# Kernel optimization log

Measured on AMD Instinct MI355X. Metric: run time of the kernel, lower is better.

## Reference

```python
import jax, jax.numpy as jnp
import numpy as np
import math

TOTAL_HEADS = 16
CONTEXTUAL_HEADS = 4


def _compute_slopes(heads):
    def slopes_power_of_2(n):
        start = 2 ** (-2 ** (-(math.log2(n) - 3)))
        ratio = start
        return [start * ratio ** i for i in range(n)]
    if math.log2(heads).is_integer():
        return slopes_power_of_2(heads)
    closest = 2 ** math.floor(math.log2(heads))
    return slopes_power_of_2(closest) + slopes_power_of_2(2 * closest)[0::2][: heads - closest]


def setup_inputs() -> dict:
    key = jax.random.key(0)
    kq, kk = jax.random.split(key)
    b, h, s, d = 1, 16, 2048, 64
    q = jax.random.normal(kq, (b, h, s, d), dtype=jnp.float32)
    k = jax.random.normal(kk, (b, h, s, d), dtype=jnp.float32)
    cross_attn_bias = jnp.zeros((TOTAL_HEADS, 1, 1), dtype=jnp.float32)
    return {"q": q, "k": k, "cross_attn_bias": cross_attn_bias,
            "i": s, "j": s, "offset": 0, "prefix": 16}


def reference(q, k, cross_attn_bias, i, j, offset, prefix):
    b = q.shape[0]
    ch = CONTEXTUAL_HEADS
    slopes = jnp.asarray(_compute_slopes(TOTAL_HEADS), dtype=jnp.float32).reshape(-1, 1, 1)  # [H,1,1]

    # base distance bias: -|j - i|, shape [i, j]
    i_arange = jnp.arange(offset, i + offset)
    j_arange = jnp.arange(j)
    bias = -jnp.abs(j_arange[None, :] - i_arange[:, None]).astype(jnp.float32)

    # contextual heads: data-dependent bias with bidirectional cumsum
    qc = q[:, :ch]
    kc = k[:, :ch]
    dots = jnp.einsum('bhid,bhjd->bhij', qc, kc) * (qc.shape[-1] ** -0.5)
    c_bias = -jax.nn.sigmoid(dots)  # [b, ch, i, j]
    upper = jnp.triu(jnp.ones((i, j), dtype=bool), offset + 1)
    lower = jnp.tril(jnp.ones((i, j), dtype=bool), offset - 1)
    c_up = jnp.cumsum(jnp.where(upper, c_bias, 0.0), axis=-1)
    c_lo = jnp.flip(jnp.cumsum(jnp.flip(jnp.where(lower, c_bias, 0.0), axis=-1), axis=-1), axis=-1)
    c_pos = c_up + c_lo  # [b, ch, i, j]

    bias_full = jnp.concatenate(
        [c_pos, jnp.broadcast_to(bias, (b, TOTAL_HEADS - ch, i, j))], axis=1)  # [b, H, i, j]

    attn_bias = slopes * bias_full  # symmetric path

    # prefix cross-attention bias
    is_prefix = jnp.arange(j) < prefix
    is_cross = (is_prefix[:, None] ^ is_prefix[None, :])[offset:]  # [i, j]
    attn_bias = jnp.where(is_cross, cross_attn_bias, attn_bias)
    return attn_bias
```

## Files before the change

kernel.cpp:

```cpp
#include <hip/hip_runtime.h>
#include <hip/hip_bf16.h>

typedef __bf16 bf16_t;
typedef bf16_t bf16x8 __attribute__((ext_vector_type(8)));
typedef float f32x4 __attribute__((ext_vector_type(4)));
typedef unsigned long long u64_t;

#define TH 16
#define CH 4
#define DD 64
#define SJ 2048
#define SP (SJ + 4)
#define RROWS 8
#define KT (SJ/16)
#define NCTX (CH*SJ/RROWS)
#define AROWS 16
#define NALIBI ((TH-CH)*SJ/AROWS)
#define NBLK (NCTX + NALIBI)
#define WSK_BYTES ((size_t)CH*KT*2*64*16)

__device__ __forceinline__ float sigmoidf_(float x) {
    return __builtin_amdgcn_rcpf(1.0f + __expf(-x));
}

__device__ __forceinline__ float bsel(u64_t u, int e) {
    return __uint_as_float((((unsigned int)(u >> (16 * e)) & 0xffffu) << 16));
}

__global__ __launch_bounds__(256) void prep_kernel(
    const float* __restrict__ k, bf16_t* __restrict__ wsk)
{
    const int t    = (int)blockIdx.x * 256 + (int)threadIdx.x;
    const int h    = t >> 14;
    const int ct   = (t >> 7) & 127;
    const int kk   = (t >> 6) & 1;
    const int lane = t & 63;
    const int col  = ct * 16 + (lane & 15);
    const int db   = kk * 32 + (lane >> 4) * 8;
    const float* p = k + ((size_t)h * SJ + col) * DD + db;
    f32x4 v0 = *(const f32x4*)p;
    f32x4 v1 = *(const f32x4*)(p + 4);
    bf16x8 o;
    #pragma unroll
    for (int e = 0; e < 4; ++e) { o[e] = (bf16_t)v0[e]; o[e + 4] = (bf16_t)v1[e]; }
    *(bf16x8*)(wsk + (size_t)t * 8) = o;
}

__global__ __launch_bounds__(512, 4) void fused_kernel(
    const float* __restrict__ q, const float* __restrict__ k,
    const bf16_t* __restrict__ wsk, int use_ws,
    const float* __restrict__ cab, const int* __restrict__ offp,
    const int* __restrict__ prep, float* __restrict__ out)
{
    __shared__ bf16_t Smb[RROWS][SP];
    __shared__ float tot[RROWS][8];
    __shared__ float pd_in[RROWS], pd_ex[RROWS];
    const int tid  = (int)threadIdx.x;
    const int lane = tid & 63;
    const int w    = tid >> 6;
    const int offset = offp[0];
    const int prefix = prep[0];
    const int bx = (int)blockIdx.x;
    const int m5 = bx % 5;

    if (m5 < 2) {
        const int id = (bx / 5) * 2 + m5;
        const int h  = id >> 8;
        const int r0 = (id & 255) * RROWS;
        const float* qh = q + (size_t)h * SJ * DD;
        const float* kh = k + (size_t)h * SJ * DD;

        bf16x8 afrag[2];
        {
            const int row   = r0 + ((lane & 15) & 7);
            const int dbase = (lane >> 4) * 8;
            const float* qp = qh + (size_t)row * DD + dbase;
            #pragma unroll
            for (int kk = 0; kk < 2; ++kk) {
                f32x4 v0 = *(const f32x4*)(qp + kk * 32);
                f32x4 v1 = *(const f32x4*)(qp + kk * 32 + 4);
                #pragma unroll
                for (int e = 0; e < 4; ++e) {
                    afrag[kk][e]     = (bf16_t)v0[e];
                    afrag[kk][e + 4] = (bf16_t)v1[e];
                }
            }
        }
        if (tid < RROWS) { pd_in[tid] = 0.f; pd_ex[tid] = 0.f; }
        const int rb = (lane >> 4) * 4;
        for (int t = 0; t < 16; ++t) {
            const int c0 = w * 256 + t * 16;
            f32x4 acc = {0.f, 0.f, 0.f, 0.f};
            if (use_ws) {
                const size_t fb = (((size_t)h * KT + (c0 >> 4)) * 2) * 64 + lane;
                #pragma unroll
                for (int kk = 0; kk < 2; ++kk) {
                    bf16x8 bfrag = *(const bf16x8*)(wsk + (fb + (size_t)kk * 64) * 8);
                    acc = __builtin_amdgcn_mfma_f32_16x16x32_bf16(afrag[kk], bfrag, acc, 0, 0, 0);
                }
            } else {
                #pragma unroll
                for (int kk = 0; kk < 2; ++kk) {
                    const int col = c0 + (lane & 15);
                    const int db  = kk * 32 + (lane >> 4) * 8;
                    const float* p = kh + (size_t)col * DD + db;
                    f32x4 v0 = *(const f32x4*)(p);
                    f32x4 v1 = *(const f32x4*)(p + 4);
                    bf16x8 bfrag;
                    #pragma unroll
                    for (int e = 0; e < 4; ++e) {
                        bfrag[e]     = (bf16_t)v0[e];
                        bfrag[e + 4] = (bf16_t)v1[e];
                    }
                    acc = __builtin_amdgcn_mfma_f32_16x16x32_bf16(afrag[kk], bfrag, acc, 0, 0, 0);
                }
            }
            if (rb < RROWS) {
                const int ccol = c0 + (lane & 15);
                #pragma unroll
                for (int m = 0; m < 4; ++m)
                    Smb[rb + m][ccol] = (bf16_t)sigmoidf_(acc[m] * 0.125f);
            }
        }
        __syncthreads();

        const float slope = exp2f(-0.5f * (float)(h + 1));
        const float cabv  = cab[h];
        const int cb = w * 256 + lane * 4;
        u64_t u[RROWS];
        float base_[RROWS];
        #pragma unroll
        for (int rl = 0; rl < RROWS; ++rl) {
            u[rl] = *(const u64_t*)(&Smb[rl][cb]);
            const float i3 = ((bsel(u[rl], 0) + bsel(u[rl], 1))
                            + (bsel(u[rl], 2) + bsel(u[rl], 3)));
            float x = i3;
            #pragma unroll
            for (int d = 1; d < 64; d <<= 1) {
                float y = __shfl_up(x, d);
                if (lane >= d) x += y;
            }
            if (lane == 63) tot[rl][w] = x;
            base_[rl] = x - i3;
        }
        __syncthreads();
        #pragma unroll
        for (int rl = 0; rl < RROWS; ++rl) {
            float b = 0.f;
            #pragma unroll
            for (int s = 0; s < 7; ++s)
                b += (s < w) ? tot[rl][s] : 0.f;
            base_[rl] += b;
            const int rg = r0 + rl, dg = rg + offset;
            const int cin = dg < SJ ? dg : SJ - 1;
            const int cex = (dg - 1) < SJ ? dg - 1 : SJ - 1;
            if (dg >= 0 && (unsigned)(cin - cb) < 4u) {
                const int e = cin - cb;
                float pi = bsel(u[rl], 0);
                if (e > 0) pi += bsel(u[rl], 1);
                if (e > 1) pi += bsel(u[rl], 2);
                if (e > 2) pi += bsel(u[rl], 3);
                pd_in[rl] = base_[rl] + pi;
            }
            if (dg >= 1 && (unsigned)(cex - cb) < 4u) {
                const int e = cex - cb;
                float pi = bsel(u[rl], 0);
                if (e > 0) pi += bsel(u[rl], 1);
                if (e > 1) pi += bsel(u[rl], 2);
                if (e > 2) pi += bsel(u[rl], 3);
                pd_ex[rl] = base_[rl] + pi;
            }
        }
        __syncthreads();
        #pragma unroll
        for (int rl = 0; rl < RROWS; ++rl) {
            const int rg = r0 + rl, dg = rg + offset;
            const float pdin = pd_in[rl];
            const float pdex = pd_ex[rl];
            const bool rpre = dg < prefix;
            const float b  = base_[rl];
            const float i0 = b  + bsel(u[rl], 0);
            const float i1 = i0 + bsel(u[rl], 1);
            const float i2 = i1 + bsel(u[rl], 2);
            const float i3 = i2 + bsel(u[rl], 3);
            const float Pc[4] = {i0, i1, i2, i3};
            const float Pm[4] = {b, i0, i1, i2};
            float* orow = out + ((size_t)h * SJ + rg) * (size_t)SJ;
            f32x4 o;
            #pragma unroll
            for (int e = 0; e < 4; ++e) {
                const int c = cb + e;
                const float cpos = (c > dg) ? -(Pc[e] - pdin)
                                 : (c < dg) ? -(pdex - Pm[e]) : 0.f;
                const bool cross = (c < prefix) != rpre;
                o[e] = cross ? cabv : slope * cpos;
            }
            *(f32x4*)(orow + cb) = o;
        }
    } else {
        const int id = (bx / 5) * 3 + (m5 - 2);
        const int h  = CH + (id >> 7);
        const int r0 = (id & 127) * AROWS;
        const float slope = exp2f(-0.5f * (float)(h + 1));
        const float cabv  = cab[h];
        #pragma unroll
        for (int rr = 0; rr < 2; ++rr) {
            const int rg = r0 + rr * 8 + w;
            const int dg = rg + offset;
            const bool rpre = dg < prefix;
            float* orow = out + ((size_t)h * SJ + rg) * (size_t)SJ;
            #pragma unroll
            for (int s = 0; s < 8; ++s) {
                const int cb = s * 256 + lane * 4;
                f32x4 o;
                #pragma unroll
                for (int e = 0; e < 4; ++e) {
                    const int c = cb + e;
                    const float v = -fabsf((float)(c - dg)) * slope;
                    const bool cross = (c < prefix) != rpre;
                    o[e] = cross ? cabv : v;
                }
                *(f32x4*)(orow + cb) = o;
            }
        }
    }
}

extern "C" void kernel_launch(void* const* d_in, const int* in_sizes, int n_in,
                              void* d_out, int out_size, void* d_ws, size_t ws_size,
                              hipStream_t stream) {
    const float* q    = (const float*)d_in[0];
    const float* k    = (const float*)d_in[1];
    const float* cab  = (const float*)d_in[2];
    const int*   offp = (const int*)d_in[5];
    const int*   prep = (const int*)d_in[6];
    float* out = (float*)d_out;
    bf16_t* wsk = (bf16_t*)d_ws;

    const int use_ws = (ws_size >= WSK_BYTES) ? 1 : 0;
    if (use_ws)
        prep_kernel<<<dim3(256), dim3(256), 0, stream>>>(k, wsk);
    fused_kernel<<<dim3(NBLK), dim3(512), 0, stream>>>(q, k, wsk, use_ws,
                                                       cab, offp, prep, out);
}
```

Before: 61.81 us.

## Merge ALiBi rows into contextual blocks and prefetch workspace B fragments

Instead of interleaving separate contextual and ALiBi blocks (2:3 by block index mod 5), every block now computes 8 contextual-head rows and then writes 24 ALiBi rows, so the grid shrinks to 1024 uniform blocks. The ALiBi stores can fill the time after the contextual scan. The workspace MFMA loop is fully unrolled and software-pipelined, loading the next B fragments before the current MFMAs run to hide global-load latency. In exchange, blocks become larger and longer, there are fewer of them for load balancing, and register pressure rises.

```diff
diff --git a/kernel.cpp b/kernel.cpp
--- a/kernel.cpp
+++ b/kernel.cpp
@@ -13,10 +13,8 @@
 #define SP (SJ + 4)
 #define RROWS 8
 #define KT (SJ/16)
-#define NCTX (CH*SJ/RROWS)
-#define AROWS 16
-#define NALIBI ((TH-CH)*SJ/AROWS)
-#define NBLK (NCTX + NALIBI)
+#define NBLK (CH*SJ/RROWS)
+#define ALPB 24
 #define WSK_BYTES ((size_t)CH*KT*2*64*16)
 
 __device__ __forceinline__ float sigmoidf_(float x) {
@@ -61,59 +59,70 @@
     const int offset = offp[0];
     const int prefix = prep[0];
     const int bx = (int)blockIdx.x;
-    const int m5 = bx % 5;
-
-    if (m5 < 2) {
-        const int id = (bx / 5) * 2 + m5;
-        const int h  = id >> 8;
-        const int r0 = (id & 255) * RROWS;
-        const float* qh = q + (size_t)h * SJ * DD;
-        const float* kh = k + (size_t)h * SJ * DD;
-
-        bf16x8 afrag[2];
-        {
-            const int row   = r0 + ((lane & 15) & 7);
-            const int dbase = (lane >> 4) * 8;
-            const float* qp = qh + (size_t)row * DD + dbase;
+
+    const int h  = bx >> 8;
+    const int r0 = (bx & 255) * RROWS;
+    const float* qh = q + (size_t)h * SJ * DD;
+    const float* kh = k + (size_t)h * SJ * DD;
+
+    bf16x8 afrag[2];
+    {
+        const int row   = r0 + ((lane & 15) & 7);
+        const int dbase = (lane >> 4) * 8;
+        const float* qp = qh + (size_t)row * DD + dbase;
+        #pragma unroll
+        for (int kk = 0; kk < 2; ++kk) {
+            f32x4 v0 = *(const f32x4*)(qp + kk * 32);
+            f32x4 v1 = *(const f32x4*)(qp + kk * 32 + 4);
             #pragma unroll
-            for (int kk = 0; kk < 2; ++kk) {
-                f32x4 v0 = *(const f32x4*)(qp + kk * 32);
-                f32x4 v1 = *(const f32x4*)(qp + kk * 32 + 4);
+            for (int e = 0; e < 4; ++e) {
+                afrag[kk][e]     = (bf16_t)v0[e];
+                afrag[kk][e + 4] = (bf16_t)v1[e];
+            }
+        }
+    }
+    if (tid < RROWS) { pd_in[tid] = 0.f; pd_ex[tid] = 0.f; }
+    const int rb = (lane >> 4) * 4;
+    if (use_ws) {
+        const bf16_t* wb = wsk + ((((size_t)h * KT + w * 16) * 2) * 64 + lane) * 8;
+        bf16x8 b0 = *(const bf16x8*)(wb);
+        bf16x8 b1 = *(const bf16x8*)(wb + 512);
+        #pragma unroll
+        for (int t = 0; t < 16; ++t) {
+            bf16x8 n0 = b0, n1 = b1;
+            if (t < 15) {
+                n0 = *(const bf16x8*)(wb + (t + 1) * 1024);
+                n1 = *(const bf16x8*)(wb + (t + 1) * 1024 + 512);
+            }
+            f32x4 acc = {0.f, 0.f, 0.f, 0.f};
+            acc = __builtin_amdgcn_mfma_f32_16x16x32_bf16(afrag[0], b0, acc, 0, 0, 0);
+            acc = __builtin_amdgcn_mfma_f32_16x16x32_bf16(afrag[1], b1, acc, 0, 0, 0);
+            if (rb < RROWS) {
+                const int ccol = w * 256 + t * 16 + (lane & 15);
                 #pragma unroll
-                for (int e = 0; e < 4; ++e) {
-                    afrag[kk][e]     = (bf16_t)v0[e];
-                    afrag[kk][e + 4] = (bf16_t)v1[e];
-                }
-            }
-        }
-        if (tid < RROWS) { pd_in[tid] = 0.f; pd_ex[tid] = 0.f; }
-        const int rb = (lane >> 4) * 4;
+                for (int m = 0; m < 4; ++m)
+                    Smb[rb + m][ccol] = (bf16_t)sigmoidf_(acc[m] * 0.125f);
+            }
+            b0 = n0; b1 = n1;
+        }
+    } else {
         for (int t = 0; t < 16; ++t) {
             const int c0 = w * 256 + t * 16;
             f32x4 acc = {0.f, 0.f, 0.f, 0.f};
-            if (use_ws) {
-                const size_t fb = (((size_t)h * KT + (c0 >> 4)) * 2) * 64 + lane;
+            #pragma unroll
+            for (int kk = 0; kk < 2; ++kk) {
+                const int col = c0 + (lane & 15);
+                const int db  = kk * 32 + (lane >> 4) * 8;
+                const float* p = kh + (size_t)col * DD + db;
+                f32x4 v0 = *(const f32x4*)(p);
+                f32x4 v1 = *(const f32x4*)(p + 4);
+                bf16x8 bfrag;
                 #pragma unroll
-                for (int kk = 0; kk < 2; ++kk) {
-                    bf16x8 bfrag = *(const bf16x8*)(wsk + (fb + (size_t)kk * 64) * 8);
-                    acc = __builtin_amdgcn_mfma_f32_16x16x32_bf16(afrag[kk], bfrag, acc, 0, 0, 0);
+                for (int e = 0; e < 4; ++e) {
+                    bfrag[e]     = (bf16_t)v0[e];
+                    bfrag[e + 4] = (bf16_t)v1[e];
                 }
-            } else {
-                #pragma unroll
-                for (int kk = 0; kk < 2; ++kk) {
-                    const int col = c0 + (lane & 15);
-                    const int db  = kk * 32 + (lane >> 4) * 8;
-                    const float* p = kh + (size_t)col * DD + db;
-                    f32x4 v0 = *(const f32x4*)(p);
-                    f32x4 v1 = *(const f32x4*)(p + 4);
-                    bf16x8 bfrag;
-                    #pragma unroll
-                    for (int e = 0; e < 4; ++e) {
-                        bfrag[e]     = (bf16_t)v0[e];
-                        bfrag[e + 4] = (bf16_t)v1[e];
-                    }
-                    acc = __builtin_amdgcn_mfma_f32_16x16x32_bf16(afrag[kk], bfrag, acc, 0, 0, 0);
-                }
+                acc = __builtin_amdgcn_mfma_f32_16x16x32_bf16(afrag[kk], bfrag, acc, 0, 0, 0);
             }
             if (rb < RROWS) {
                 const int ccol = c0 + (lane & 15);
@@ -122,106 +131,107 @@
                     Smb[rb + m][ccol] = (bf16_t)sigmoidf_(acc[m] * 0.125f);
             }
         }
-        __syncthreads();
-
-        const float slope = exp2f(-0.5f * (float)(h + 1));
-        const float cabv  = cab[h];
-        const int cb = w * 256 + lane * 4;
-        u64_t u[RROWS];
-        float base_[RROWS];
-        #pragma unroll
-        for (int rl = 0; rl < RROWS; ++rl) {
-            u[rl] = *(const u64_t*)(&Smb[rl][cb]);
-            const float i3 = ((bsel(u[rl], 0) + bsel(u[rl], 1))
-                            + (bsel(u[rl], 2) + bsel(u[rl], 3)));
-            float x = i3;
-            #pragma unroll
-            for (int d = 1; d < 64; d <<= 1) {
-                float y = __shfl_up(x, d);
-                if (lane >= d) x += y;
-            }
-            if (lane == 63) tot[rl][w] = x;
-            base_[rl] = x - i3;
-        }
-        __syncthreads();
-        #pragma unroll
-        for (int rl = 0; rl < RROWS; ++rl) {
-            float b = 0.f;
-            #pragma unroll
-            for (int s = 0; s < 7; ++s)
-                b += (s < w) ? tot[rl][s] : 0.f;
-            base_[rl] += b;
-            const int rg = r0 + rl, dg = rg + offset;
-            const int cin = dg < SJ ? dg : SJ - 1;
-            const int cex = (dg - 1) < SJ ? dg - 1 : SJ - 1;
-            if (dg >= 0 && (unsigned)(cin - cb) < 4u) {
-                const int e = cin - cb;
-                float pi = bsel(u[rl], 0);
-                if (e > 0) pi += bsel(u[rl], 1);
-                if (e > 1) pi += bsel(u[rl], 2);
-                if (e > 2) pi += bsel(u[rl], 3);
-                pd_in[rl] = base_[rl] + pi;
-            }
-            if (dg >= 1 && (unsigned)(cex - cb) < 4u) {
-                const int e = cex - cb;
-                float pi = bsel(u[rl], 0);
-                if (e > 0) pi += bsel(u[rl], 1);
-                if (e > 1) pi += bsel(u[rl], 2);
-                if (e > 2) pi += bsel(u[rl], 3);
-                pd_ex[rl] = base_[rl] + pi;
-            }
-        }
-        __syncthreads();
-        #pragma unroll
-        for (int rl = 0; rl < RROWS; ++rl) {
-            const int rg = r0 + rl, dg = rg + offset;
-            const float pdin = pd_in[rl];
-            const float pdex = pd_ex[rl];
-            const bool rpre = dg < prefix;
-            const float b  = base_[rl];
-            const float i0 = b  + bsel(u[rl], 0);
-            const float i1 = i0 + bsel(u[rl], 1);
-            const float i2 = i1 + bsel(u[rl], 2);
-            const float i3 = i2 + bsel(u[rl], 3);
-            const float Pc[4] = {i0, i1, i2, i3};
-            const float Pm[4] = {b, i0, i1, i2};
-            float* orow = out + ((size_t)h * SJ + rg) * (size_t)SJ;
+    }
+    __syncthreads();
+
+    const float slope = exp2f(-0.5f * (float)(h + 1));
+    const float cabv  = cab[h];
+    const int cb = w * 256 + lane * 4;
+    u64_t u[RROWS];
+    float base_[RROWS];
+    #pragma unroll
+    for (int rl = 0; rl < RROWS; ++rl) {
+        u[rl] = *(const u64_t*)(&Smb[rl][cb]);
+        const float i3 = ((bsel(u[rl], 0) + bsel(u[rl], 1))
+                        + (bsel(u[rl], 2) + bsel(u[rl], 3)));
+        float x = i3;
+        #pragma unroll
+        for (int d = 1; d < 64; d <<= 1) {
+            float y = __shfl_up(x, d);
+            if (lane >= d) x += y;
+        }
+        if (lane == 63) tot[rl][w] = x;
+        base_[rl] = x - i3;
+    }
+    __syncthreads();
+    #pragma unroll
+    for (int rl = 0; rl < RROWS; ++rl) {
+        float b = 0.f;
+        #pragma unroll
+        for (int s = 0; s < 7; ++s)
+            b += (s < w) ? tot[rl][s] : 0.f;
+        base_[rl] += b;
+        const int rg = r0 + rl, dg = rg + offset;
+        const int cin = dg < SJ ? dg : SJ - 1;
+        const int cex = (dg - 1) < SJ ? dg - 1 : SJ - 1;
+        if (dg >= 0 && (unsigned)(cin - cb) < 4u) {
+            const int e = cin - cb;
+            float pi = bsel(u[rl], 0);
+            if (e > 0) pi += bsel(u[rl], 1);
+            if (e > 1) pi += bsel(u[rl], 2);
+            if (e > 2) pi += bsel(u[rl], 3);
+            pd_in[rl] = base_[rl] + pi;
+        }
+        if (dg >= 1 && (unsigned)(cex - cb) < 4u) {
+            const int e = cex - cb;
+            float pi = bsel(u[rl], 0);
+            if (e > 0) pi += bsel(u[rl], 1);
+            if (e > 1) pi += bsel(u[rl], 2);
+            if (e > 2) pi += bsel(u[rl], 3);
+            pd_ex[rl] = base_[rl] + pi;
+        }
+    }
+    __syncthreads();
+
+    #pragma unroll
+    for (int rl = 0; rl < RROWS; ++rl) {
+        const int rg = r0 + rl, dg = rg + offset;
+        const float pdin = pd_in[rl];
+        const float pdex = pd_ex[rl];
+        const bool rpre = dg < prefix;
+        const float b  = base_[rl];
+        const float i0 = b  + bsel(u[rl], 0);
+        const float i1 = i0 + bsel(u[rl], 1);
+        const float i2 = i1 + bsel(u[rl], 2);
+        const float i3 = i2 + bsel(u[rl], 3);
+        const float Pc[4] = {i0, i1, i2, i3};
+        const float Pm[4] = {b, i0, i1, i2};
+        float* orow = out + ((size_t)h * SJ + rg) * (size_t)SJ;
+        f32x4 o;
+        #pragma unroll
+        for (int e = 0; e < 4; ++e) {
+            const int c = cb + e;
+            const float cpos = (c > dg) ? -(Pc[e] - pdin)
+                             : (c < dg) ? -(pdex - Pm[e]) : 0.f;
+            const bool cross = (c < prefix) != rpre;
+            o[e] = cross ? cabv : slope * cpos;
+        }
+        *(f32x4*)(orow + cb) = o;
+    }
+
+    const int R0 = bx * ALPB;
+    #pragma unroll
+    for (int rr = 0; rr < 3; ++rr) {
+        const int R  = R0 + rr * 8 + w;
+        const int ha = CH + (R >> 11);
+        const int r  = R & (SJ - 1);
+        const int dg = r + offset;
+        const float sl = exp2f(-0.5f * (float)(ha + 1));
+        const float cv = cab[ha];
+        const bool rpre = dg < prefix;
+        float* orow = out + ((size_t)ha * SJ + r) * (size_t)SJ;
+        #pragma unroll
+        for (int s = 0; s < 8; ++s) {
+            const int cba = s * 256 + lane * 4;
             f32x4 o;
             #pragma unroll
             for (int e = 0; e < 4; ++e) {
-                const int c = cb + e;
-                const float cpos = (c > dg) ? -(Pc[e] - pdin)
-                                 : (c < dg) ? -(pdex - Pm[e]) : 0.f;
+                const int c = cba + e;
+                const float v = -fabsf((float)(c - dg)) * sl;
                 const bool cross = (c < prefix) != rpre;
-                o[e] = cross ? cabv : slope * cpos;
-            }
-            *(f32x4*)(orow + cb) = o;
-        }
-    } else {
-        const int id = (bx / 5) * 3 + (m5 - 2);
-        const int h  = CH + (id >> 7);
-        const int r0 = (id & 127) * AROWS;
-        const float slope = exp2f(-0.5f * (float)(h + 1));
-        const float cabv  = cab[h];
-        #pragma unroll
-        for (int rr = 0; rr < 2; ++rr) {
-            const int rg = r0 + rr * 8 + w;
-            const int dg = rg + offset;
-            const bool rpre = dg < prefix;
-            float* orow = out + ((size_t)h * SJ + rg) * (size_t)SJ;
-            #pragma unroll
-            for (int s = 0; s < 8; ++s) {
-                const int cb = s * 256 + lane * 4;
-                f32x4 o;
-                #pragma unroll
-                for (int e = 0; e < 4; ++e) {
-                    const int c = cb + e;
-                    const float v = -fabsf((float)(c - dg)) * slope;
-                    const bool cross = (c < prefix) != rpre;
-                    o[e] = cross ? cabv : v;
-                }
-                *(f32x4*)(orow + cb) = o;
-            }
+                o[e] = cross ? cv : v;
+            }
+            *(f32x4*)(orow + cba) = o;
         }
     }
 }
```

Result: slower. 67.93 us (+9.9%).
